# Optimization experiments

Hardware: AMD Instinct MI355X
Metric: run time of the kernel (lower is better)

The kernel has to match this reference:

```python
import jax, jax.numpy as jnp
import numpy as np
from jax import lax

BS, L, HID = 16, 512, 768
H, HD, NREG = 12, 64, 8
R2 = 2 * NREG


def setup_inputs() -> dict:
    key = jax.random.key(0)
    ks = jax.random.split(key, 7)
    s = 1.0 / np.sqrt(HID)
    return {
        "hidden_states": jax.random.normal(ks[0], (BS, L, HID), jnp.float32),
        "K1_w": jax.random.normal(ks[1], (H * HD, HID), jnp.float32) * s,
        "K1_b": jnp.zeros((H * HD,), jnp.float32),
        "V1_w": jax.random.normal(ks[2], (H * HD, HID), jnp.float32) * s,
        "V1_b": jnp.zeros((H * HD,), jnp.float32),
        "reading_head": jax.random.normal(ks[3], (H, HD), jnp.float32) * (1.0 / np.sqrt(HD)),
        "bidirection_weight": jnp.ones((1, 1, H, 1, R2), jnp.float32) * (1.0 / R2),
    }


def _softmax_dim1(x):
    # torch: softmax over length dim (1) plus 1/exp(max) residual term
    m = jnp.max(x, axis=1, keepdims=True)
    e = jnp.exp(x - m)
    return e / jnp.sum(e, axis=1, keepdims=True) + jnp.exp(-m)


def _cummax_idx(e):
    # torch.cummax indices over axis=1 for a bool tensor (ties -> latest index):
    # last True index so far; if no True yet, current index.
    ar = jnp.arange(e.shape[1], dtype=jnp.int32)[None, :, None]
    lt = lax.cummax(jnp.where(e, ar, jnp.int32(-1)), axis=1)
    return jnp.where(lt >= 0, lt, ar)


def reference(hidden_states, K1_w, K1_b, V1_w, V1_b, reading_head, bidirection_weight):
    bs, length, _ = hidden_states.shape
    K1 = jax.nn.relu(hidden_states @ K1_w.T + K1_b).reshape(bs, length, H, HD)
    V1 = jax.nn.relu(hidden_states @ V1_w.T + V1_b).reshape(bs, length, H, HD)

    scores = jnp.einsum("blhn,hn->blh", K1, reading_head)
    events = _softmax_dim1(scores) > (1.5 / length)  # (bs, L, H) bool; fwd==bwd for IC1

    col0 = _cummax_idx(events)  # (bs, L, H)
    rolled = jnp.roll(events, -1, axis=1)
    col1 = jnp.flip(512 - _cummax_idx(jnp.flip(rolled, axis=1)), axis=1)
    col1 = col1.at[:, 0].set(0)

    # sequential shift-register scan over length
    e_seq = jnp.moveaxis(events, 1, 0)  # (L, bs, H)
    f_seq = jnp.moveaxis(col0, 1, 0)
    b_seq = jnp.moveaxis(col1, 1, 0)
    row0 = jnp.concatenate(
        [f_seq[0][:, None], b_seq[0][:, None], jnp.zeros((bs, R2, H), jnp.int32)], axis=1
    )  # (bs, R2+2, H)

    def step(row, inp):
        e, f, b = inp
        reg = jnp.where(e[:, None, :], row[:, :-2], row[:, 2:])  # shift-in on event
        new_row = jnp.concatenate([f[:, None], b[:, None], reg], axis=1)
        return new_row, reg

    _, regs = lax.scan(step, row0, (e_seq[1:], f_seq[1:], b_seq[1:]))
    regs = jnp.concatenate([jnp.zeros((1, bs, R2, H), jnp.int32), regs], axis=0)  # (L,bs,R2,H)
    idx = jnp.moveaxis(regs, 0, 1).reshape(bs, length * R2, H)
    idx = jnp.clip(idx, 0, length - 1)

    V2 = jnp.take_along_axis(V1, idx[..., None], axis=1).reshape(bs, length, R2, H, HD)
    w = bidirection_weight.reshape(H, R2)
    return jnp.einsum("blrhd,hr->blhd", V2, w)  # (bs, L, H, HD)
```

## Files before the change

### kernel.cpp

```cpp
#include <hip/hip_runtime.h>
#include <cstdint>
#include <cstddef>

#define BSZ 16
#define LQ  512
#define HIDDIM 768
#define NH  12
#define HD  64
#define R2V 16
#define NTOT 1536
#define MTOT 8192

typedef __bf16 bf16x8 __attribute__((ext_vector_type(8)));
typedef float  f32x4  __attribute__((ext_vector_type(4)));

__device__ inline unsigned short f2bf(float x) {
    union { float f; unsigned u; } c; c.f = x;
    unsigned r = c.u + 0x7fffu + ((c.u >> 16) & 1u);
    return (unsigned short)(r >> 16);
}
__device__ inline float bfl(unsigned u) { return __uint_as_float(u << 16); }
__device__ inline float bfh(unsigned u) { return __uint_as_float(u & 0xffff0000u); }

#define NHS4 1572864
#define NW1  147456
#define NW4  294912

__global__ __launch_bounds__(256) void cast_pack(
    const float* __restrict__ hs,
    const float* __restrict__ Kw, const float* __restrict__ Vw,
    const float* __restrict__ Kb, const float* __restrict__ Vb,
    unsigned short* __restrict__ hsb, unsigned short* __restrict__ Wb,
    float* __restrict__ biasp)
{
    const int i = blockIdx.x * 256 + threadIdx.x;
    float4 v; unsigned short* dst;
    if (i < NHS4) {
        v = ((const float4*)hs)[i];
        dst = hsb + (size_t)i * 4;
    } else {
        const int j = i - NHS4;
        v = (j < NW1) ? ((const float4*)Kw)[j] : ((const float4*)Vw)[j - NW1];
        dst = Wb + (size_t)j * 4;
    }
    ushort4 o;
    o.x = f2bf(v.x); o.y = f2bf(v.y); o.z = f2bf(v.z); o.w = f2bf(v.w);
    *(ushort4*)dst = o;
    if (i < 768) { biasp[i] = Kb[i]; biasp[768 + i] = Vb[i]; }
}

#define TBM 128
#define TBN 64
#define TBK 32
#define KITERS (HIDDIM / TBK)

#define GLD16(g, l) __builtin_amdgcn_global_load_lds( \
    (const __attribute__((address_space(1))) void*)(g), \
    (__attribute__((address_space(3))) void*)(l), 16, 0, 0)

__global__ __launch_bounds__(256) void gemm_mfma(
    const unsigned short* __restrict__ Abf,
    const unsigned short* __restrict__ Wbf,
    const float* __restrict__ biasp,
    unsigned short* __restrict__ K1b,
    float* __restrict__ V1f)
{
    __shared__ unsigned short As[2][TBM * TBK];
    __shared__ unsigned short Bs[2][TBN * TBK];

    const int n0   = blockIdx.x * TBN;
    const int m0   = blockIdx.y * TBM;
    const int tid  = threadIdx.x;
    const int wid  = tid >> 6;
    const int lane = tid & 63;
    const int wm   = (wid & 1) * 64;
    const int wn   = (wid >> 1) * 32;

    f32x4 acc[4][2] = {};

    const int rA = wid * 32 + (lane >> 2);
    const int kp = (lane & 3) * 8;
    const unsigned short* Ap0 = Abf + (size_t)(m0 + rA) * HIDDIM + kp;
    const unsigned short* Ap1 = Abf + (size_t)(m0 + rA + 16) * HIDDIM + kp;
    const int rB = wid * 16 + (lane >> 2);
    const unsigned short* Bp0 = Wbf + (size_t)(n0 + rB) * HIDDIM + kp;

#define STAGE(buf, kof)                                            \
    do {                                                           \
        GLD16(Ap0 + (kof), &As[buf][(wid * 32) * TBK]);            \
        GLD16(Ap1 + (kof), &As[buf][(wid * 32 + 16) * TBK]);       \
        GLD16(Bp0 + (kof), &Bs[buf][(wid * 16) * TBK]);            \
    } while (0)

    const int fm = lane & 15;
    const int fk = (lane >> 4) * 8;

    STAGE(0, 0);

    for (int it = 0; it < KITERS; ++it) {
        __syncthreads();
        const int cb = it & 1;
        if (it + 1 < KITERS) STAGE(cb ^ 1, (it + 1) * TBK);

        bf16x8 af[4], bfr[2];
        #pragma unroll
        for (int mi = 0; mi < 4; ++mi)
            af[mi] = *reinterpret_cast<const bf16x8*>(&As[cb][(wm + mi * 16 + fm) * TBK + fk]);
        #pragma unroll
        for (int ni = 0; ni < 2; ++ni)
            bfr[ni] = *reinterpret_cast<const bf16x8*>(&Bs[cb][(wn + ni * 16 + fm) * TBK + fk]);
        #pragma unroll
        for (int mi = 0; mi < 4; ++mi)
            #pragma unroll
            for (int ni = 0; ni < 2; ++ni)
                acc[mi][ni] = __builtin_amdgcn_mfma_f32_16x16x32_bf16(
                    bfr[ni], af[mi], acc[mi][ni], 0, 0, 0);
    }
#undef STAGE

    const bool isK = (n0 < HIDDIM);
    const int ncol0 = isK ? n0 : (n0 - HIDDIM);
    const int mloc = lane & 15;
    const int nq   = (lane >> 4) * 4;

    if (isK) {
        #pragma unroll
        for (int mi = 0; mi < 4; ++mi) {
            const int mg = m0 + wm + mi * 16 + mloc;
            #pragma unroll
            for (int ni = 0; ni < 2; ++ni) {
                const int col = ncol0 + wn + ni * 16 + nq;
                float4 bv = *(const float4*)(biasp + (isK ? 0 : HIDDIM) + col);
                f32x4 a = acc[mi][ni];
                ushort4 o;
                o.x = f2bf(fmaxf(a[0] + bv.x, 0.f));
                o.y = f2bf(fmaxf(a[1] + bv.y, 0.f));
                o.z = f2bf(fmaxf(a[2] + bv.z, 0.f));
                o.w = f2bf(fmaxf(a[3] + bv.w, 0.f));
                *(ushort4*)(K1b + (size_t)mg * HIDDIM + col) = o;
            }
        }
    } else {
        #pragma unroll
        for (int mi = 0; mi < 4; ++mi) {
            const int mg = m0 + wm + mi * 16 + mloc;
            #pragma unroll
            for (int ni = 0; ni < 2; ++ni) {
                const int col = ncol0 + wn + ni * 16 + nq;
                float4 bv = *(const float4*)(biasp + HIDDIM + col);
                f32x4 a = acc[mi][ni];
                float4 o;
                o.x = fmaxf(a[0] + bv.x, 0.f);
                o.y = fmaxf(a[1] + bv.y, 0.f);
                o.z = fmaxf(a[2] + bv.z, 0.f);
                o.w = fmaxf(a[3] + bv.w, 0.f);
                *(float4*)(V1f + (size_t)mg * HIDDIM + col) = o;
            }
        }
    }
}

#define SINF (1 << 30)
#define IXP 17

__global__ __launch_bounds__(512) void scan_gather(
    const unsigned short* __restrict__ K1b,
    const float* __restrict__ V1f,
    const float* __restrict__ rh,
    const float* __restrict__ bw,
    float* __restrict__ out)
{
    const int bh   = blockIdx.x;
    const int b    = bh / NH;
    const int h    = bh % NH;
    const int l    = threadIdx.x;
    const int lane = l & 63;
    const int wid  = l >> 6;

    __shared__ float wredA[8];
    __shared__ float wredB[8];
    __shared__ int   wp0[8];
    __shared__ int   wp1[8];
    __shared__ int   wp2[8];
    __shared__ int   ev[LQ];
    __shared__ int   col0[LQ];
    __shared__ int   col1[LQ];
    __shared__ int   E[LQ];
    __shared__ int   idxs[LQ * IXP];
    __shared__ float wsm[R2V];

    if (l < R2V) wsm[l] = bw[h * R2V + l];

    const unsigned short* krow = K1b + ((size_t)(b * LQ + l)) * HIDDIM + h * HD;
    const float* rrow = rh + h * HD;
    float s = 0.f;
    #pragma unroll
    for (int c8 = 0; c8 < 8; ++c8) {
        uint4 kv = *(const uint4*)(krow + c8 * 8);
        float4 ra = *(const float4*)(rrow + c8 * 8);
        float4 rb = *(const float4*)(rrow + c8 * 8 + 4);
        s += bfl(kv.x) * ra.x + bfh(kv.x) * ra.y
           + bfl(kv.y) * ra.z + bfh(kv.y) * ra.w
           + bfl(kv.z) * rb.x + bfh(kv.z) * rb.y
           + bfl(kv.w) * rb.z + bfh(kv.w) * rb.w;
    }

    float mx = s;
    #pragma unroll
    for (int off = 32; off > 0; off >>= 1) mx = fmaxf(mx, __shfl_xor(mx, off));
    if (lane == 0) wredA[wid] = mx;
    __syncthreads();
    float m = wredA[0];
    #pragma unroll
    for (int i = 1; i < 8; ++i) m = fmaxf(m, wredA[i]);

    const float e = expf(s - m);
    float sm = e;
    #pragma unroll
    for (int off = 32; off > 0; off >>= 1) sm += __shfl_xor(sm, off);
    if (lane == 0) wredB[wid] = sm;
    __syncthreads();
    float ssum = 0.f;
    #pragma unroll
    for (int i = 0; i < 8; ++i) ssum += wredB[i];

    const float p = e / ssum + expf(-m);
    const int event = (p > (1.5f / 512.0f)) ? 1 : 0;
    ev[l] = event;

    int v = event ? l : -1;
    #pragma unroll
    for (int off = 1; off < 64; off <<= 1) {
        int u = __shfl_up(v, off);
        if (lane >= off) v = (u > v) ? u : v;
    }
    if (lane == 63) wp0[wid] = v;
    __syncthreads();
    int pfx = -1;
    for (int i = 0; i < wid; ++i) pfx = (wp0[i] > pfx) ? wp0[i] : pfx;
    v = (pfx > v) ? pfx : v;
    col0[l] = (v >= 0) ? v : l;

    int v1 = ev[(l + 1) & (LQ - 1)] ? l : SINF;
    #pragma unroll
    for (int off = 1; off < 64; off <<= 1) {
        int u = __shfl_down(v1, off);
        if (lane < 64 - off) v1 = (u < v1) ? u : v1;
    }
    if (lane == 0) wp1[wid] = v1;
    __syncthreads();
    int sfx = SINF;
    for (int i = wid + 1; i < 8; ++i) sfx = (wp1[i] < sfx) ? wp1[i] : sfx;
    v1 = (sfx < v1) ? sfx : v1;
    col1[l] = (l == 0) ? 0 : (((v1 < SINF) ? v1 : l) + 1);

    int c = (l >= 1) ? event : 0;
    #pragma unroll
    for (int off = 1; off < 64; off <<= 1) {
        int u = __shfl_up(c, off);
        if (lane >= off) c += u;
    }
    if (lane == 63) wp2[wid] = c;
    __syncthreads();
    for (int i = 0; i < wid; ++i) c += wp2[i];

    if (l >= 1 && event) E[c - 1] = l;
    __syncthreads();

    int* op = &idxs[l * IXP];
    #pragma unroll
    for (int j = 0; j < 8; ++j) {
        const int k = c - 1 - j;
        int f = 0, bb = 0;
        if (k >= 0) {
            const int t = E[k];
            f  = col0[t - 1];
            bb = col1[t - 1];
        }
        op[2 * j]     = min(max(f, 0), LQ - 1);
        op[2 * j + 1] = min(max(bb, 0), LQ - 1);
    }
    __syncthreads();

    const int dsl = lane & 7;
    const size_t vbase = (size_t)b * LQ * HIDDIM + h * HD + dsl * 8;

    for (int round = 0; round < 8; ++round) {
        const int lg = round * 64 + wid * 8 + (lane >> 3);
        const int* ip = &idxs[lg * IXP];
        float4 accA = make_float4(0.f, 0.f, 0.f, 0.f);
        float4 accB = make_float4(0.f, 0.f, 0.f, 0.f);
        #pragma unroll 1
        for (int rc = 0; rc < R2V; rc += 4) {
            const int i0 = ip[rc], i1 = ip[rc + 1], i2 = ip[rc + 2], i3 = ip[rc + 3];
            const float w0 = wsm[rc], w1 = wsm[rc + 1], w2 = wsm[rc + 2], w3 = wsm[rc + 3];
            const float* p0 = V1f + vbase + (size_t)i0 * HIDDIM;
            const float* p1 = V1f + vbase + (size_t)i1 * HIDDIM;
            const float* p2 = V1f + vbase + (size_t)i2 * HIDDIM;
            const float* p3 = V1f + vbase + (size_t)i3 * HIDDIM;
            float4 a0 = *(const float4*)p0, b0 = *(const float4*)(p0 + 4);
            float4 a1 = *(const float4*)p1, b1 = *(const float4*)(p1 + 4);
            float4 a2 = *(const float4*)p2, b2 = *(const float4*)(p2 + 4);
            float4 a3 = *(const float4*)p3, b3 = *(const float4*)(p3 + 4);
            accA.x += w0 * a0.x + w1 * a1.x + w2 * a2.x + w3 * a3.x;
            accA.y += w0 * a0.y + w1 * a1.y + w2 * a2.y + w3 * a3.y;
            accA.z += w0 * a0.z + w1 * a1.z + w2 * a2.z + w3 * a3.z;
            accA.w += w0 * a0.w + w1 * a1.w + w2 * a2.w + w3 * a3.w;
            accB.x += w0 * b0.x + w1 * b1.x + w2 * b2.x + w3 * b3.x;
            accB.y += w0 * b0.y + w1 * b1.y + w2 * b2.y + w3 * b3.y;
            accB.z += w0 * b0.z + w1 * b1.z + w2 * b2.z + w3 * b3.z;
            accB.w += w0 * b0.w + w1 * b1.w + w2 * b2.w + w3 * b3.w;
        }
        float* po = out + ((size_t)(b * LQ + lg) * NH + h) * HD + dsl * 8;
        *(float4*)po       = accA;
        *((float4*)po + 1) = accB;
    }
}

extern "C" void kernel_launch(void* const* d_in, const int* in_sizes, int n_in,
                              void* d_out, int out_size, void* d_ws, size_t ws_size,
                              hipStream_t stream)
{
    (void)in_sizes; (void)n_in; (void)out_size; (void)ws_size;

    const float* hs = (const float*)d_in[0];
    const float* Kw = (const float*)d_in[1];
    const float* Kb = (const float*)d_in[2];
    const float* Vw = (const float*)d_in[3];
    const float* Vb = (const float*)d_in[4];
    const float* rh = (const float*)d_in[5];
    const float* bw = (const float*)d_in[6];
    float* out = (float*)d_out;

    char* ws = (char*)d_ws;
    unsigned short* K1b   = (unsigned short*)(ws);
    float*          V1f   = (float*)(ws + 12582912);
    unsigned short* hsb   = (unsigned short*)(ws + 37748736);
    unsigned short* Wb    = (unsigned short*)(ws + 50331648);
    float*          biasp = (float*)(ws + 52690944);

    cast_pack<<<(NHS4 + NW4) / 256, 256, 0, stream>>>(hs, Kw, Vw, Kb, Vb, hsb, Wb, biasp);

    dim3 g1(NTOT / TBN, MTOT / TBM);
    gemm_mfma<<<g1, 256, 0, stream>>>(hsb, Wb, biasp, K1b, V1f);

    scan_gather<<<BSZ * NH, LQ, 0, stream>>>(K1b, V1f, rh, bw, out);
}
```

Before: 156.4 us.

## Fuse reading-head score reduction into GEMM epilogue and widen N tile

The K-projection epilogue now computes each row's dot product with the reading head directly from the accumulators. It reduces across lanes and writes one float score per (head, row) instead of storing the full bf16 K1 matrix. The GEMM N tile grows from 64 to 128 so that each warp covers exactly one 64-wide head, which makes the in-register reduction possible. This removes the K1 write and re-read and shrinks the workspace. In exchange the accumulator count doubles, raising register pressure, and the grid halves, which lowers the number of blocks in flight.

```diff
diff --git a/kernel.cpp b/kernel.cpp
--- a/kernel.cpp
+++ b/kernel.cpp
@@ -19,8 +19,6 @@
     unsigned r = c.u + 0x7fffu + ((c.u >> 16) & 1u);
     return (unsigned short)(r >> 16);
 }
-__device__ inline float bfl(unsigned u) { return __uint_as_float(u << 16); }
-__device__ inline float bfh(unsigned u) { return __uint_as_float(u & 0xffff0000u); }
 
 #define NHS4 1572864
 #define NW1  147456
@@ -50,7 +48,7 @@
 }
 
 #define TBM 128
-#define TBN 64
+#define TBN 128
 #define TBK 32
 #define KITERS (HIDDIM / TBK)
 
@@ -62,7 +60,8 @@
     const unsigned short* __restrict__ Abf,
     const unsigned short* __restrict__ Wbf,
     const float* __restrict__ biasp,
-    unsigned short* __restrict__ K1b,
+    const float* __restrict__ rh,
+    float* __restrict__ scores,
     float* __restrict__ V1f)
 {
     __shared__ unsigned short As[2][TBM * TBK];
@@ -74,22 +73,25 @@
     const int wid  = tid >> 6;
     const int lane = tid & 63;
     const int wm   = (wid & 1) * 64;
-    const int wn   = (wid >> 1) * 32;
-
-    f32x4 acc[4][2] = {};
-
-    const int rA = wid * 32 + (lane >> 2);
+    const int wn   = (wid >> 1) * 64;
+
+    f32x4 acc[4][4] = {};
+
+    const int r0 = wid * 32;
+    const int rA = r0 + (lane >> 2);
     const int kp = (lane & 3) * 8;
+
     const unsigned short* Ap0 = Abf + (size_t)(m0 + rA) * HIDDIM + kp;
     const unsigned short* Ap1 = Abf + (size_t)(m0 + rA + 16) * HIDDIM + kp;
-    const int rB = wid * 16 + (lane >> 2);
-    const unsigned short* Bp0 = Wbf + (size_t)(n0 + rB) * HIDDIM + kp;
-
-#define STAGE(buf, kof)                                            \
-    do {                                                           \
-        GLD16(Ap0 + (kof), &As[buf][(wid * 32) * TBK]);            \
-        GLD16(Ap1 + (kof), &As[buf][(wid * 32 + 16) * TBK]);       \
-        GLD16(Bp0 + (kof), &Bs[buf][(wid * 16) * TBK]);            \
+    const unsigned short* Bp0 = Wbf + (size_t)(n0 + rA) * HIDDIM + kp;
+    const unsigned short* Bp1 = Wbf + (size_t)(n0 + rA + 16) * HIDDIM + kp;
+
+#define STAGE(buf, kof)                                        \
+    do {                                                       \
+        GLD16(Ap0 + (kof), &As[buf][r0 * TBK]);                \
+        GLD16(Ap1 + (kof), &As[buf][(r0 + 16) * TBK]);         \
+        GLD16(Bp0 + (kof), &Bs[buf][r0 * TBK]);                \
+        GLD16(Bp1 + (kof), &Bs[buf][(r0 + 16) * TBK]);         \
     } while (0)
 
     const int fm = lane & 15;
@@ -102,50 +104,57 @@
         const int cb = it & 1;
         if (it + 1 < KITERS) STAGE(cb ^ 1, (it + 1) * TBK);
 
-        bf16x8 af[4], bfr[2];
+        bf16x8 af[4], bfr[4];
         #pragma unroll
         for (int mi = 0; mi < 4; ++mi)
             af[mi] = *reinterpret_cast<const bf16x8*>(&As[cb][(wm + mi * 16 + fm) * TBK + fk]);
         #pragma unroll
-        for (int ni = 0; ni < 2; ++ni)
+        for (int ni = 0; ni < 4; ++ni)
             bfr[ni] = *reinterpret_cast<const bf16x8*>(&Bs[cb][(wn + ni * 16 + fm) * TBK + fk]);
         #pragma unroll
         for (int mi = 0; mi < 4; ++mi)
             #pragma unroll
-            for (int ni = 0; ni < 2; ++ni)
+            for (int ni = 0; ni < 4; ++ni)
                 acc[mi][ni] = __builtin_amdgcn_mfma_f32_16x16x32_bf16(
                     bfr[ni], af[mi], acc[mi][ni], 0, 0, 0);
     }
 #undef STAGE
 
     const bool isK = (n0 < HIDDIM);
-    const int ncol0 = isK ? n0 : (n0 - HIDDIM);
     const int mloc = lane & 15;
     const int nq   = (lane >> 4) * 4;
 
     if (isK) {
+        const int h = (n0 + wn) >> 6;
+        float4 rhv[4], bvv[4];
+        #pragma unroll
+        for (int ni = 0; ni < 4; ++ni) {
+            rhv[ni] = *(const float4*)(rh + h * HD + ni * 16 + nq);
+            bvv[ni] = *(const float4*)(biasp + n0 + wn + ni * 16 + nq);
+        }
+        #pragma unroll
+        for (int mi = 0; mi < 4; ++mi) {
+            float s = 0.f;
+            #pragma unroll
+            for (int ni = 0; ni < 4; ++ni) {
+                f32x4 a = acc[mi][ni];
+                s += fmaxf(a[0] + bvv[ni].x, 0.f) * rhv[ni].x
+                   + fmaxf(a[1] + bvv[ni].y, 0.f) * rhv[ni].y
+                   + fmaxf(a[2] + bvv[ni].z, 0.f) * rhv[ni].z
+                   + fmaxf(a[3] + bvv[ni].w, 0.f) * rhv[ni].w;
+            }
+            s += __shfl_xor(s, 16);
+            s += __shfl_xor(s, 32);
+            if (lane < 16)
+                scores[(size_t)h * MTOT + m0 + wm + mi * 16 + lane] = s;
+        }
+    } else {
+        const int ncol0 = n0 - HIDDIM;
         #pragma unroll
         for (int mi = 0; mi < 4; ++mi) {
             const int mg = m0 + wm + mi * 16 + mloc;
             #pragma unroll
-            for (int ni = 0; ni < 2; ++ni) {
-                const int col = ncol0 + wn + ni * 16 + nq;
-                float4 bv = *(const float4*)(biasp + (isK ? 0 : HIDDIM) + col);
-                f32x4 a = acc[mi][ni];
-                ushort4 o;
-                o.x = f2bf(fmaxf(a[0] + bv.x, 0.f));
-                o.y = f2bf(fmaxf(a[1] + bv.y, 0.f));
-                o.z = f2bf(fmaxf(a[2] + bv.z, 0.f));
-                o.w = f2bf(fmaxf(a[3] + bv.w, 0.f));
-                *(ushort4*)(K1b + (size_t)mg * HIDDIM + col) = o;
-            }
-        }
-    } else {
-        #pragma unroll
-        for (int mi = 0; mi < 4; ++mi) {
-            const int mg = m0 + wm + mi * 16 + mloc;
-            #pragma unroll
-            for (int ni = 0; ni < 2; ++ni) {
+            for (int ni = 0; ni < 4; ++ni) {
                 const int col = ncol0 + wn + ni * 16 + nq;
                 float4 bv = *(const float4*)(biasp + HIDDIM + col);
                 f32x4 a = acc[mi][ni];
@@ -164,9 +173,8 @@
 #define IXP 17
 
 __global__ __launch_bounds__(512) void scan_gather(
-    const unsigned short* __restrict__ K1b,
+    const float* __restrict__ scores,
     const float* __restrict__ V1f,
-    const float* __restrict__ rh,
     const float* __restrict__ bw,
     float* __restrict__ out)
 {
@@ -191,19 +199,7 @@
 
     if (l < R2V) wsm[l] = bw[h * R2V + l];
 
-    const unsigned short* krow = K1b + ((size_t)(b * LQ + l)) * HIDDIM + h * HD;
-    const float* rrow = rh + h * HD;
-    float s = 0.f;
-    #pragma unroll
-    for (int c8 = 0; c8 < 8; ++c8) {
-        uint4 kv = *(const uint4*)(krow + c8 * 8);
-        float4 ra = *(const float4*)(rrow + c8 * 8);
-        float4 rb = *(const float4*)(rrow + c8 * 8 + 4);
-        s += bfl(kv.x) * ra.x + bfh(kv.x) * ra.y
-           + bfl(kv.y) * ra.z + bfh(kv.y) * ra.w
-           + bfl(kv.z) * rb.x + bfh(kv.z) * rb.y
-           + bfl(kv.w) * rb.z + bfh(kv.w) * rb.w;
-    }
+    const float s = scores[(size_t)h * MTOT + b * LQ + l];
 
     float mx = s;
     #pragma unroll
@@ -333,16 +329,16 @@
     float* out = (float*)d_out;
 
     char* ws = (char*)d_ws;
-    unsigned short* K1b   = (unsigned short*)(ws);
-    float*          V1f   = (float*)(ws + 12582912);
-    unsigned short* hsb   = (unsigned short*)(ws + 37748736);
-    unsigned short* Wb    = (unsigned short*)(ws + 50331648);
-    float*          biasp = (float*)(ws + 52690944);
+    float*          V1f    = (float*)(ws);
+    unsigned short* hsb    = (unsigned short*)(ws + 25165824);
+    unsigned short* Wb     = (unsigned short*)(ws + 37748736);
+    float*          biasp  = (float*)(ws + 40108032);
+    float*          scores = (float*)(ws + 40114176);
 
     cast_pack<<<(NHS4 + NW4) / 256, 256, 0, stream>>>(hs, Kw, Vw, Kb, Vb, hsb, Wb, biasp);
 
     dim3 g1(NTOT / TBN, MTOT / TBM);
-    gemm_mfma<<<g1, 256, 0, stream>>>(hsb, Wb, biasp, K1b, V1f);
-
-    scan_gather<<<BSZ * NH, LQ, 0, stream>>>(K1b, V1f, rh, bw, out);
-}
+    gemm_mfma<<<g1, 256, 0, stream>>>(hsb, Wb, biasp, rh, scores, V1f);
+
+    scan_gather<<<BSZ * NH, LQ, 0, stream>>>(scores, V1f, bw, out);
+}
```

Result: no change. 157.2 us (+0.5%).
